# Performance work log

Hardware: AMD Instinct MI355X
Metric: run time of the kernel (lower is better)

## Reference

```python
import jax, jax.numpy as jnp
import numpy as np

B, T, N_EMBD = 1, 512, 768
N_HEAD, N_KV_HEAD = 12, 6
HEAD_DIM = N_EMBD // N_HEAD  # 64


def rms_norm(x, eps=1e-6):
    return x * jax.lax.rsqrt(jnp.mean(x * x, axis=-1, keepdims=True) + eps)


def apply_rotary_emb(x, cos, sin):
    # x: [B, T, H, D]; cos/sin: [T, D//2]
    d2 = x.shape[-1] // 2
    x1, x2 = x[..., :d2], x[..., d2:]
    c = cos[None, :, None, :]
    s = sin[None, :, None, :]
    return jnp.concatenate([x1 * c - x2 * s, x2 * c + x1 * s], axis=-1)


def tropical_dot_product(q, k):
    # q: [B,H,T,D], k: [B,H,S,D] -> max-plus score [B,H,T,S]
    return jnp.max(q[..., :, None, :] + k[..., None, :, :], axis=-1)


def setup_inputs() -> dict:
    key = jax.random.key(0)
    ks = jax.random.split(key, 5)
    x = jax.random.normal(ks[0], (B, T, N_EMBD), dtype=jnp.float32)
    # Real RoPE tables
    half = HEAD_DIM // 2
    inv_freq = 1.0 / (10000.0 ** (np.arange(0, half, dtype=np.float32) / half))
    t = np.arange(T, dtype=np.float32)
    freqs = np.outer(t, inv_freq)  # [T, D//2]
    cos = jnp.asarray(np.cos(freqs), dtype=jnp.float32)
    sin = jnp.asarray(np.sin(freqs), dtype=jnp.float32)
    std = 0.02
    Wq = std * jax.random.normal(ks[1], (N_EMBD, N_HEAD * HEAD_DIM), dtype=jnp.float32)
    Wk = std * jax.random.normal(ks[2], (N_EMBD, N_KV_HEAD * HEAD_DIM), dtype=jnp.float32)
    Wv = std * jax.random.normal(ks[3], (N_EMBD, N_KV_HEAD * HEAD_DIM), dtype=jnp.float32)
    Wproj = std * jax.random.normal(ks[4], (N_EMBD, N_EMBD), dtype=jnp.float32)
    return {"x": x, "cos": cos, "sin": sin, "Wq": Wq, "Wk": Wk, "Wv": Wv, "Wproj": Wproj}


def reference(x, cos, sin, Wq, Wk, Wv, Wproj):
    b, t, c = x.shape
    q = (x @ Wq).reshape(b, t, N_HEAD, HEAD_DIM)
    k = (x @ Wk).reshape(b, t, N_KV_HEAD, HEAD_DIM)
    v = (x @ Wv).reshape(b, t, N_KV_HEAD, HEAD_DIM)
    q = rms_norm(apply_rotary_emb(q, cos, sin))
    k = rms_norm(apply_rotary_emb(k, cos, sin))
    q = jnp.transpose(q, (0, 2, 1, 3))  # [B,H,T,D]
    k = jnp.transpose(k, (0, 2, 1, 3))  # [B,Hkv,T,D]
    v = jnp.transpose(v, (0, 2, 1, 3))
    n_rep = N_HEAD // N_KV_HEAD
    if n_rep > 1:
        k = jnp.repeat(k, n_rep, axis=1)
        v = jnp.repeat(v, n_rep, axis=1)
    scores = tropical_dot_product(q, k)  # [B,H,T,T]
    causal = jnp.tril(jnp.ones((t, t), dtype=jnp.bool_))
    scores = scores + jnp.where(causal, 0.0, -jnp.inf)
    attn = jax.nn.softmax(scores, axis=-1)
    y = jnp.einsum('bhqk,bhkd->bhqd', attn, v)
    y = jnp.transpose(y, (0, 2, 1, 3)).reshape(b, t, c)
    return y @ Wproj
```

## Files before the change

kernel.cpp:

```cpp
#include <hip/hip_runtime.h>
#include <hip/hip_bf16.h>
#include <math.h>

#define TT   512
#define CEMB 768
#define NH   12
#define NKV  6
#define HD   64
#define KVC  (NKV*HD)

typedef short short8 __attribute__((ext_vector_type(8)));
typedef float floatx4 __attribute__((ext_vector_type(4)));

__device__ __forceinline__ unsigned pack_bf16(float lo, float hi){
  __hip_bfloat162 h = __float22bfloat162_rn(make_float2(lo, hi));
  return *reinterpret_cast<unsigned*>(&h);
}
__device__ __forceinline__ unsigned short bf16_rn(float f){
  unsigned u = __float_as_uint(f);
  u += 0x7FFFu + ((u>>16)&1u);
  return (unsigned short)(u>>16);
}
__device__ __forceinline__ float bf16_to_f32(unsigned short u){
  return __uint_as_float(((unsigned)u) << 16);
}

__global__ void __launch_bounds__(256) gemm_qkv_mfma(
    const float* __restrict__ X,
    const float* __restrict__ Wq, const float* __restrict__ Wk, const float* __restrict__ Wv,
    const float* __restrict__ Wp,
    const float* __restrict__ cosb, const float* __restrict__ sinb,
    float* __restrict__ q, float* __restrict__ k, float* __restrict__ v,
    unsigned short* __restrict__ WpF){
  int bx = blockIdx.x;
  if (bx >= 192){
    int t0 = (bx-192)*256 + threadIdx.x;
    for(int g=0; g<8; ++g){
      int u  = g*9216 + t0;
      int kp = u / 192;
      int n4 = (u - kp*192)*4;
      int kk = kp*2;
      float4 w0 = *(const float4*)&Wp[(size_t)kk*CEMB + n4];
      float4 w1 = *(const float4*)&Wp[(size_t)(kk+1)*CEMB + n4];
      int ks = kk>>5, qq = (kk>>3)&3, j = kk&7;
      #pragma unroll
      for(int i=0;i<4;i++){
        int n = n4+i, ct = n>>4, r = n&15;
        *(unsigned*)&WpF[ (((size_t)(ct*24 + ks)*64 + qq*16 + r)<<3) + j ] =
          pack_bf16((&w0.x)[i], (&w1.x)[i]);
      }
    }
    return;
  }
  int mt = bx / 24, nt = bx % 24;
  const float* W; int ldb, bcol;
  if (nt < 12)      { W = Wq; ldb = CEMB; bcol = nt*64; }
  else if (nt < 18) { W = Wk; ldb = KVC;  bcol = (nt-12)*64; }
  else              { W = Wv; ldb = KVC;  bcol = (nt-18)*64; }

  __shared__ __align__(16) unsigned short Al[2][64][40];
  __shared__ __align__(16) unsigned short Bl[2][64][40];

  int tid = threadIdx.x;
  int am  = tid>>2,  akg = (tid&3)*8;
  int bkp = tid>>4,  bn4 = (tid&15)*4;
  int w = tid>>6, lane = tid&63, qq = lane>>4, r = lane&15;

  floatx4 acc[4];
  #pragma unroll
  for(int c=0;c<4;c++) acc[c] = (floatx4){0.f,0.f,0.f,0.f};

  const float* Ap = X + (size_t)(mt*64 + am)*CEMB + akg;
  const float* Bp = W + (size_t)(2*bkp)*ldb + bcol + bn4;

  float4 a0 = *(const float4*)(Ap);
  float4 a1 = *(const float4*)(Ap + 4);
  float4 b0 = *(const float4*)(Bp);
  float4 b1 = *(const float4*)(Bp + ldb);

  int buf = 0;
  for(int k0=0; k0<CEMB; k0+=32){
    unsigned p0 = pack_bf16(a0.x,a0.y), p1 = pack_bf16(a0.z,a0.w);
    unsigned p2 = pack_bf16(a1.x,a1.y), p3 = pack_bf16(a1.z,a1.w);
    *(uint4*)&Al[buf][am][akg] = make_uint4(p0,p1,p2,p3);
    #pragma unroll
    for(int i=0;i<4;i++)
      *(unsigned*)&Bl[buf][bn4+i][2*bkp] = pack_bf16((&b0.x)[i], (&b1.x)[i]);
    if (k0 + 32 < CEMB){
      a0 = *(const float4*)(Ap + k0+32);
      a1 = *(const float4*)(Ap + k0+36);
      b0 = *(const float4*)(Bp + (size_t)(k0+32)*ldb);
      b1 = *(const float4*)(Bp + (size_t)(k0+33)*ldb);
    }
    __syncthreads();
    short8 af = *(short8*)&Al[buf][w*16 + r][qq*8];
    #pragma unroll
    for(int c=0;c<4;c++){
      short8 bf = *(short8*)&Bl[buf][c*16 + r][qq*8];
      acc[c] = __builtin_amdgcn_mfma_f32_16x16x32_bf16(af, bf, acc[c], 0,0,0);
    }
    buf ^= 1;
  }

  #pragma unroll
  for(int reg=0; reg<4; ++reg){
    int t = mt*64 + w*16 + qq*4 + reg;
    if (nt < 18){
      float cs0 = cosb[t*32 + r],      sn0 = sinb[t*32 + r];
      float cs1 = cosb[t*32 + 16 + r], sn1 = sinb[t*32 + 16 + r];
      float x0 = acc[0][reg], x1 = acc[1][reg], x2 = acc[2][reg], x3 = acc[3][reg];
      float n0 = x0*cs0 - x2*sn0;
      float n1 = x1*cs1 - x3*sn1;
      float n2 = x2*cs0 + x0*sn0;
      float n3 = x3*cs1 + x1*sn1;
      float ss = n0*n0 + n1*n1 + n2*n2 + n3*n3;
      ss += __shfl_xor(ss,1); ss += __shfl_xor(ss,2);
      ss += __shfl_xor(ss,4); ss += __shfl_xor(ss,8);
      float sc = rsqrtf(ss*(1.0f/64.0f) + 1e-6f);
      float* dst = (nt < 12) ? (q + (size_t)t*CEMB + nt*64)
                             : (k + (size_t)t*KVC + (nt-12)*64);
      dst[r]    = n0*sc; dst[16+r] = n1*sc;
      dst[32+r] = n2*sc; dst[48+r] = n3*sc;
    } else {
      float* dst = v + (size_t)t*KVC + (nt-18)*64;
      dst[r]    = acc[0][reg]; dst[16+r] = acc[1][reg];
      dst[32+r] = acc[2][reg]; dst[48+r] = acc[3][reg];
    }
  }
}

__global__ void __launch_bounds__(256) attn_tile(const float* __restrict__ qn,
    const float* __restrict__ kn, const float* __restrict__ vr,
    unsigned short* __restrict__ part_acc, float2* __restrict__ part_ml){
  __shared__ float QPsh[64*68];
  __shared__ float Ksh[64*64];
  __shared__ float Vsh[64*64];

  int h   = blockIdx.y;
  int idx = blockIdx.x;
  int qt = 0, rem = idx;
  while (rem > qt){ rem -= (qt+1); ++qt; }
  int ct = rem;
  int t0 = ct*64;

  int kvh  = h >> 1;
  int w    = threadIdx.x >> 6;
  int lane = threadIdx.x & 63;
  int lg   = lane >> 4;
  int lc   = lane & 15;

  #pragma unroll
  for(int sub=0; sub<4; ++sub){
    int rr = w*16 + sub*4 + lg;
    int sw = ((lc ^ (rr>>2)) & 15)*4;
    *(float4*)&QPsh[rr*68 + lc*4] =
      *(const float4*)&qn[(size_t)(qt*64+rr)*CEMB + h*HD + lc*4];
    *(float4*)&Ksh[rr*64 + sw] =
      *(const float4*)&kn[(size_t)(t0+rr)*KVC + kvh*HD + lc*4];
    *(float4*)&Vsh[rr*64 + sw] =
      *(const float4*)&vr[(size_t)(t0+rr)*KVC + kvh*HD + lc*4];
  }
  __syncthreads();

  float s[4][4];
  #pragma unroll
  for(int r=0;r<4;r++)
    #pragma unroll
    for(int c=0;c<4;c++) s[r][c] = -INFINITY;

  #pragma unroll
  for(int dg=0; dg<16; ++dg){
    float4 k4[4], q4[4];
    int ksw = ((dg ^ lc)&15)*4;
    #pragma unroll
    for(int c=0;c<4;c++)
      k4[c] = *(const float4*)&Ksh[(lc*4+c)*64 + ksw];
    #pragma unroll
    for(int r=0;r<4;r++)
      q4[r] = *(const float4*)&QPsh[(w*16+lg*4+r)*68 + dg*4];
    #pragma unroll
    for(int r=0;r<4;r++)
      #pragma unroll
      for(int c=0;c<4;c++)
        s[r][c] = fmaxf(s[r][c],
                  fmaxf(fmaxf(q4[r].x + k4[c].x, q4[r].y + k4[c].y),
                        fmaxf(q4[r].z + k4[c].z, q4[r].w + k4[c].w)));
  }

  float mrow[4], lrow[4];
  #pragma unroll
  for(int r=0;r<4;r++){
    int i = qt*64 + w*16 + lg*4 + r;
    #pragma unroll
    for(int c=0;c<4;c++)
      if (t0 + lc*4 + c > i) s[r][c] = -INFINITY;
    float mt = fmaxf(fmaxf(s[r][0],s[r][1]), fmaxf(s[r][2],s[r][3]));
    mt = fmaxf(mt, __shfl_xor(mt,1));
    mt = fmaxf(mt, __shfl_xor(mt,2));
    mt = fmaxf(mt, __shfl_xor(mt,4));
    mt = fmaxf(mt, __shfl_xor(mt,8));
    float p0 = __expf(s[r][0]-mt), p1 = __expf(s[r][1]-mt);
    float p2 = __expf(s[r][2]-mt), p3 = __expf(s[r][3]-mt);
    float ps = p0+p1+p2+p3;
    ps += __shfl_xor(ps,1); ps += __shfl_xor(ps,2);
    ps += __shfl_xor(ps,4); ps += __shfl_xor(ps,8);
    mrow[r] = mt; lrow[r] = ps;
    *(float4*)&QPsh[(w*16+lg*4+r)*68 + lc*4] = make_float4(p0,p1,p2,p3);
  }
  __builtin_amdgcn_wave_barrier();

  float acc[4][4];
  #pragma unroll
  for(int r=0;r<4;r++)
    #pragma unroll
    for(int c=0;c<4;c++) acc[r][c] = 0.f;

  #pragma unroll
  for(int jg=0; jg<16; ++jg){
    float4 v4[4], p4[4];
    int vsw = ((lc ^ jg)&15)*4;
    #pragma unroll
    for(int jj=0;jj<4;jj++)
      v4[jj] = *(const float4*)&Vsh[(jg*4+jj)*64 + vsw];
    #pragma unroll
    for(int r=0;r<4;r++)
      p4[r] = *(const float4*)&QPsh[(w*16+lg*4+r)*68 + jg*4];
    #pragma unroll
    for(int r=0;r<4;r++)
      #pragma unroll
      for(int c=0;c<4;c++)
        acc[r][c] = fmaf(p4[r].x, (&v4[0].x)[c], fmaf(p4[r].y, (&v4[1].x)[c],
                    fmaf(p4[r].z, (&v4[2].x)[c], fmaf(p4[r].w, (&v4[3].x)[c], acc[r][c]))));
  }

  #pragma unroll
  for(int r=0;r<4;r++){
    int i = qt*64 + w*16 + lg*4 + r;
    int pidx = (h*TT + i)*8 + ct;
    *(uint2*)&part_acc[(size_t)pidx*64 + lc*4] =
      make_uint2(pack_bf16(acc[r][0],acc[r][1]), pack_bf16(acc[r][2],acc[r][3]));
    if (lc == 0) part_ml[pidx] = make_float2(mrow[r], lrow[r]);
  }
}

__global__ void __launch_bounds__(256) attn_reduce(const unsigned short* __restrict__ part_acc,
    const float2* __restrict__ part_ml, unsigned short* __restrict__ yF){
  int wid  = (blockIdx.x * blockDim.x + threadIdx.x) >> 6;
  int lane = threadIdx.x & 63;
  int h = wid >> 9;
  int i = wid & 511;
  int nch = (i >> 6) + 1;
  int base = (h*TT + i)*8;

  float2 mls[8]; float acs[8];
  #pragma unroll
  for(int c=0;c<8;c++){
    mls[c] = part_ml[base + c];
    acs[c] = bf16_to_f32(part_acc[(size_t)(base + c)*64 + lane]);
  }

  float m = -INFINITY, l = 0.f, a = 0.f;
  #pragma unroll
  for(int c=0;c<8;c++){
    if (c < nch){
      float m_new = fmaxf(m, mls[c].x);
      float sa  = __expf(m - m_new);
      float sc_ = __expf(mls[c].x - m_new);
      l = l*sa + mls[c].y*sc_;
      a = a*sa + acs[c]*sc_;
      m = m_new;
    }
  }
  float val = a / l;
  int s = i>>4, rr = i&15;
  int ks = h*2 + (lane>>5), q2 = (lane>>3)&3, j = lane&7;
  yF[ (((size_t)(s*24 + ks)*64 + q2*16 + rr)<<3) + j ] = bf16_rn(val);
}

__global__ void __launch_bounds__(256) gemm_proj_mfma(
    const unsigned short* __restrict__ yF, const unsigned short* __restrict__ WpF,
    float* __restrict__ out){
  int bx = blockIdx.x;
  int mt = bx / 24, ntH = bx % 24;
  int tid = threadIdx.x, w = tid>>6, lane = tid&63, qq = lane>>4, r = lane&15;
  int s = mt*4 + w;

  const short8* Af = (const short8*)yF  + (size_t)s*24*64 + lane;
  const short8* Bf = (const short8*)WpF + lane;

  floatx4 acc[2];
  acc[0] = (floatx4){0.f,0.f,0.f,0.f};
  acc[1] = (floatx4){0.f,0.f,0.f,0.f};

  short8 ac_ = Af[0];
  short8 bc_[2];
  #pragma unroll
  for(int c=0;c<2;c++) bc_[c] = Bf[(size_t)((ntH*2+c)*24)*64];

  for(int ks=0; ks<24; ++ks){
    short8 an; short8 bn[2];
    if (ks < 23){
      an = Af[(size_t)(ks+1)*64];
      #pragma unroll
      for(int c=0;c<2;c++) bn[c] = Bf[(size_t)((ntH*2+c)*24 + ks+1)*64];
    }
    #pragma unroll
    for(int c=0;c<2;c++)
      acc[c] = __builtin_amdgcn_mfma_f32_16x16x32_bf16(ac_, bc_[c], acc[c], 0,0,0);
    if (ks < 23){
      ac_ = an;
      #pragma unroll
      for(int c=0;c<2;c++) bc_[c] = bn[c];
    }
  }

  #pragma unroll
  for(int reg=0; reg<4; ++reg){
    int t = mt*64 + w*16 + qq*4 + reg;
    float* dst = out + (size_t)t*CEMB + ntH*32;
    #pragma unroll
    for(int c=0;c<2;c++)
      dst[c*16 + r] = acc[c][reg];
  }
}

extern "C" void kernel_launch(void* const* d_in, const int* in_sizes, int n_in,
                              void* d_out, int out_size, void* d_ws, size_t ws_size,
                              hipStream_t stream){
  const float* x    = (const float*)d_in[0];
  const float* cosb = (const float*)d_in[1];
  const float* sinb = (const float*)d_in[2];
  const float* Wq   = (const float*)d_in[3];
  const float* Wk   = (const float*)d_in[4];
  const float* Wv   = (const float*)d_in[5];
  const float* Wp   = (const float*)d_in[6];
  float* out = (float*)d_out;

  float* ws        = (float*)d_ws;
  float* q_raw     = ws;
  float* k_raw     = q_raw + (size_t)TT*CEMB;
  float* v_raw     = k_raw + (size_t)TT*KVC;
  unsigned short* part_acc = (unsigned short*)(v_raw + (size_t)TT*KVC);
  float2* part_ml  = (float2*)(part_acc + (size_t)NH*TT*8*64);
  unsigned short* WpF = (unsigned short*)(part_ml + (size_t)NH*TT*8);
  unsigned short* yF  = WpF + (size_t)48*24*64*8;

  gemm_qkv_mfma <<<dim3(228),   256, 0, stream>>>(x, Wq, Wk, Wv, Wp, cosb, sinb,
                                                  q_raw, k_raw, v_raw, WpF);
  attn_tile     <<<dim3(36,NH), 256, 0, stream>>>(q_raw, k_raw, v_raw, part_acc, part_ml);
  attn_reduce   <<<dim3(NH*TT/4), 256, 0, stream>>>(part_acc, part_ml, yF);
  gemm_proj_mfma<<<dim3(192),   256, 0, stream>>>(yF, WpF, out);
}
```

Measured before the change: 115.8 us.

## Split attention tiles to 32 query rows, use packed float2 math, deepen GEMM prefetch

The attention tile kernel now handles 32 query rows per block instead of 64, doubling the grid to 72x12 blocks for more parallelism on the causal triangle. It also rewrites the inner max-plus and PV loops with float2 vector types to encourage packed FP32 instructions. The QKV GEMM unrolls its double-buffered loop into two explicit steps with two register prefetch sets in flight. The projection GEMM gets a 3-deep register prefetch ring. The risks are reduced per-block work, which means more K/V reloads per query, and higher register pressure.

Result: no change. 116.1 us (+0.3%).

```diff
diff --git a/kernel.cpp b/kernel.cpp
--- a/kernel.cpp
+++ b/kernel.cpp
@@ -11,6 +11,7 @@
 
 typedef short short8 __attribute__((ext_vector_type(8)));
 typedef float floatx4 __attribute__((ext_vector_type(4)));
+typedef float floatx2 __attribute__((ext_vector_type(2)));
 
 __device__ __forceinline__ unsigned pack_bf16(float lo, float hi){
   __hip_bfloat162 h = __float22bfloat162_rn(make_float2(lo, hi));
@@ -73,33 +74,41 @@
   const float* Ap = X + (size_t)(mt*64 + am)*CEMB + akg;
   const float* Bp = W + (size_t)(2*bkp)*ldb + bcol + bn4;
 
-  float4 a0 = *(const float4*)(Ap);
-  float4 a1 = *(const float4*)(Ap + 4);
-  float4 b0 = *(const float4*)(Bp);
-  float4 b1 = *(const float4*)(Bp + ldb);
-
-  int buf = 0;
-  for(int k0=0; k0<CEMB; k0+=32){
-    unsigned p0 = pack_bf16(a0.x,a0.y), p1 = pack_bf16(a0.z,a0.w);
-    unsigned p2 = pack_bf16(a1.x,a1.y), p3 = pack_bf16(a1.z,a1.w);
-    *(uint4*)&Al[buf][am][akg] = make_uint4(p0,p1,p2,p3);
+  float4 a00 = *(const float4*)(Ap);
+  float4 a01 = *(const float4*)(Ap + 4);
+  float4 b00 = *(const float4*)(Bp);
+  float4 b01 = *(const float4*)(Bp + ldb);
+  float4 a10 = *(const float4*)(Ap + 32);
+  float4 a11 = *(const float4*)(Ap + 36);
+  float4 b10 = *(const float4*)(Bp + (size_t)32*ldb);
+  float4 b11 = *(const float4*)(Bp + (size_t)33*ldb);
+
+  auto step = [&](int k0, float4& A0, float4& A1, float4& B0, float4& B1,
+                  int bufc) {
+    unsigned p0 = pack_bf16(A0.x,A0.y), p1 = pack_bf16(A0.z,A0.w);
+    unsigned p2 = pack_bf16(A1.x,A1.y), p3 = pack_bf16(A1.z,A1.w);
+    *(uint4*)&Al[bufc][am][akg] = make_uint4(p0,p1,p2,p3);
     #pragma unroll
     for(int i=0;i<4;i++)
-      *(unsigned*)&Bl[buf][bn4+i][2*bkp] = pack_bf16((&b0.x)[i], (&b1.x)[i]);
-    if (k0 + 32 < CEMB){
-      a0 = *(const float4*)(Ap + k0+32);
-      a1 = *(const float4*)(Ap + k0+36);
-      b0 = *(const float4*)(Bp + (size_t)(k0+32)*ldb);
-      b1 = *(const float4*)(Bp + (size_t)(k0+33)*ldb);
+      *(unsigned*)&Bl[bufc][bn4+i][2*bkp] = pack_bf16((&B0.x)[i], (&B1.x)[i]);
+    if (k0 + 64 < CEMB){
+      A0 = *(const float4*)(Ap + k0+64);
+      A1 = *(const float4*)(Ap + k0+68);
+      B0 = *(const float4*)(Bp + (size_t)(k0+64)*ldb);
+      B1 = *(const float4*)(Bp + (size_t)(k0+65)*ldb);
     }
     __syncthreads();
-    short8 af = *(short8*)&Al[buf][w*16 + r][qq*8];
+    short8 af = *(short8*)&Al[bufc][w*16 + r][qq*8];
     #pragma unroll
     for(int c=0;c<4;c++){
-      short8 bf = *(short8*)&Bl[buf][c*16 + r][qq*8];
-      acc[c] = __builtin_amdgcn_mfma_f32_16x16x32_bf16(af, bf, acc[c], 0,0,0);
-    }
-    buf ^= 1;
+      short8 bfr = *(short8*)&Bl[bufc][c*16 + r][qq*8];
+      acc[c] = __builtin_amdgcn_mfma_f32_16x16x32_bf16(af, bfr, acc[c], 0,0,0);
+    }
+  };
+
+  for(int k0=0; k0<CEMB; k0+=64){
+    step(k0,    a00,a01,b00,b01, 0);
+    step(k0+32, a10,a11,b10,b11, 1);
   }
 
   #pragma unroll
@@ -132,29 +141,36 @@
 __global__ void __launch_bounds__(256) attn_tile(const float* __restrict__ qn,
     const float* __restrict__ kn, const float* __restrict__ vr,
     unsigned short* __restrict__ part_acc, float2* __restrict__ part_ml){
-  __shared__ float QPsh[64*68];
+  __shared__ float QPsh[32*68];
   __shared__ float Ksh[64*64];
   __shared__ float Vsh[64*64];
 
   int h   = blockIdx.y;
   int idx = blockIdx.x;
-  int qt = 0, rem = idx;
-  while (rem > qt){ rem -= (qt+1); ++qt; }
+  int qs = 0, rem = idx;
+  while (rem > (qs>>1)){ rem -= (qs>>1)+1; ++qs; }
   int ct = rem;
   int t0 = ct*64;
 
   int kvh  = h >> 1;
-  int w    = threadIdx.x >> 6;
-  int lane = threadIdx.x & 63;
+  int tid  = threadIdx.x;
+  int w    = tid >> 6;
+  int lane = tid & 63;
   int lg   = lane >> 4;
   int lc   = lane & 15;
 
+  {
+    int rr = tid >> 4;
+    int c4 = (tid & 15) * 4;
+    *(float4*)&QPsh[rr*68 + c4] =
+      *(const float4*)&qn[(size_t)(qs*32+rr)*CEMB + h*HD + c4];
+    *(float4*)&QPsh[(rr+16)*68 + c4] =
+      *(const float4*)&qn[(size_t)(qs*32+rr+16)*CEMB + h*HD + c4];
+  }
   #pragma unroll
   for(int sub=0; sub<4; ++sub){
     int rr = w*16 + sub*4 + lg;
     int sw = ((lc ^ (rr>>2)) & 15)*4;
-    *(float4*)&QPsh[rr*68 + lc*4] =
-      *(const float4*)&qn[(size_t)(qt*64+rr)*CEMB + h*HD + lc*4];
     *(float4*)&Ksh[rr*64 + sw] =
       *(const float4*)&kn[(size_t)(t0+rr)*KVC + kvh*HD + lc*4];
     *(float4*)&Vsh[rr*64 + sw] =
@@ -162,35 +178,41 @@
   }
   __syncthreads();
 
-  float s[4][4];
-  #pragma unroll
-  for(int r=0;r<4;r++)
+  float s[2][4];
+  #pragma unroll
+  for(int r=0;r<2;r++)
     #pragma unroll
     for(int c=0;c<4;c++) s[r][c] = -INFINITY;
 
   #pragma unroll
   for(int dg=0; dg<16; ++dg){
-    float4 k4[4], q4[4];
+    floatx2 ka[4], kb[4];
     int ksw = ((dg ^ lc)&15)*4;
     #pragma unroll
-    for(int c=0;c<4;c++)
-      k4[c] = *(const float4*)&Ksh[(lc*4+c)*64 + ksw];
-    #pragma unroll
-    for(int r=0;r<4;r++)
-      q4[r] = *(const float4*)&QPsh[(w*16+lg*4+r)*68 + dg*4];
-    #pragma unroll
-    for(int r=0;r<4;r++)
+    for(int c=0;c<4;c++){
+      float4 kv = *(const float4*)&Ksh[(lc*4+c)*64 + ksw];
+      ka[c] = (floatx2){kv.x, kv.y};
+      kb[c] = (floatx2){kv.z, kv.w};
+    }
+    #pragma unroll
+    for(int r=0;r<2;r++){
+      float4 qv = *(const float4*)&QPsh[(w*8+lg*2+r)*68 + dg*4];
+      floatx2 qa = (floatx2){qv.x, qv.y};
+      floatx2 qb = (floatx2){qv.z, qv.w};
       #pragma unroll
-      for(int c=0;c<4;c++)
+      for(int c=0;c<4;c++){
+        floatx2 sa = qa + ka[c];
+        floatx2 sb = qb + kb[c];
         s[r][c] = fmaxf(s[r][c],
-                  fmaxf(fmaxf(q4[r].x + k4[c].x, q4[r].y + k4[c].y),
-                        fmaxf(q4[r].z + k4[c].z, q4[r].w + k4[c].w)));
-  }
-
-  float mrow[4], lrow[4];
-  #pragma unroll
-  for(int r=0;r<4;r++){
-    int i = qt*64 + w*16 + lg*4 + r;
+                  fmaxf(fmaxf(sa.x, sa.y), fmaxf(sb.x, sb.y)));
+      }
+    }
+  }
+
+  float mrow[2], lrow[2];
+  #pragma unroll
+  for(int r=0;r<2;r++){
+    int i = qs*32 + w*8 + lg*2 + r;
     #pragma unroll
     for(int c=0;c<4;c++)
       if (t0 + lc*4 + c > i) s[r][c] = -INFINITY;
@@ -205,40 +227,47 @@
     ps += __shfl_xor(ps,1); ps += __shfl_xor(ps,2);
     ps += __shfl_xor(ps,4); ps += __shfl_xor(ps,8);
     mrow[r] = mt; lrow[r] = ps;
-    *(float4*)&QPsh[(w*16+lg*4+r)*68 + lc*4] = make_float4(p0,p1,p2,p3);
+    *(float4*)&QPsh[(w*8+lg*2+r)*68 + lc*4] = make_float4(p0,p1,p2,p3);
   }
   __builtin_amdgcn_wave_barrier();
 
-  float acc[4][4];
-  #pragma unroll
-  for(int r=0;r<4;r++)
-    #pragma unroll
-    for(int c=0;c<4;c++) acc[r][c] = 0.f;
+  floatx2 acc2[2][2];
+  #pragma unroll
+  for(int r=0;r<2;r++){
+    acc2[r][0] = (floatx2){0.f,0.f};
+    acc2[r][1] = (floatx2){0.f,0.f};
+  }
 
   #pragma unroll
   for(int jg=0; jg<16; ++jg){
-    float4 v4[4], p4[4];
+    floatx2 va[4], vb[4];
     int vsw = ((lc ^ jg)&15)*4;
     #pragma unroll
-    for(int jj=0;jj<4;jj++)
-      v4[jj] = *(const float4*)&Vsh[(jg*4+jj)*64 + vsw];
-    #pragma unroll
-    for(int r=0;r<4;r++)
-      p4[r] = *(const float4*)&QPsh[(w*16+lg*4+r)*68 + jg*4];
-    #pragma unroll
-    for(int r=0;r<4;r++)
+    for(int jj=0;jj<4;jj++){
+      float4 vv = *(const float4*)&Vsh[(jg*4+jj)*64 + vsw];
+      va[jj] = (floatx2){vv.x, vv.y};
+      vb[jj] = (floatx2){vv.z, vv.w};
+    }
+    #pragma unroll
+    for(int r=0;r<2;r++){
+      float4 pv = *(const float4*)&QPsh[(w*8+lg*2+r)*68 + jg*4];
       #pragma unroll
-      for(int c=0;c<4;c++)
-        acc[r][c] = fmaf(p4[r].x, (&v4[0].x)[c], fmaf(p4[r].y, (&v4[1].x)[c],
-                    fmaf(p4[r].z, (&v4[2].x)[c], fmaf(p4[r].w, (&v4[3].x)[c], acc[r][c]))));
-  }
-
-  #pragma unroll
-  for(int r=0;r<4;r++){
-    int i = qt*64 + w*16 + lg*4 + r;
+      for(int jj=0;jj<4;jj++){
+        float pj = (&pv.x)[jj];
+        floatx2 pp = (floatx2){pj, pj};
+        acc2[r][0] = __builtin_elementwise_fma(pp, va[jj], acc2[r][0]);
+        acc2[r][1] = __builtin_elementwise_fma(pp, vb[jj], acc2[r][1]);
+      }
+    }
+  }
+
+  #pragma unroll
+  for(int r=0;r<2;r++){
+    int i = qs*32 + w*8 + lg*2 + r;
     int pidx = (h*TT + i)*8 + ct;
     *(uint2*)&part_acc[(size_t)pidx*64 + lc*4] =
-      make_uint2(pack_bf16(acc[r][0],acc[r][1]), pack_bf16(acc[r][2],acc[r][3]));
+      make_uint2(pack_bf16(acc2[r][0].x, acc2[r][0].y),
+                 pack_bf16(acc2[r][1].x, acc2[r][1].y));
     if (lc == 0) part_ml[pidx] = make_float2(mrow[r], lrow[r]);
   }
 }
@@ -292,26 +321,26 @@
   acc[0] = (floatx4){0.f,0.f,0.f,0.f};
   acc[1] = (floatx4){0.f,0.f,0.f,0.f};
 
-  short8 ac_ = Af[0];
-  short8 bc_[2];
-  #pragma unroll
-  for(int c=0;c<2;c++) bc_[c] = Bf[(size_t)((ntH*2+c)*24)*64];
-
+  short8 ar[4]; short8 br[4][2];
+  #pragma unroll
+  for(int j=0;j<3;++j){
+    ar[j] = Af[(size_t)j*64];
+    #pragma unroll
+    for(int c=0;c<2;c++) br[j][c] = Bf[(size_t)((ntH*2+c)*24 + j)*64];
+  }
+
+  #pragma unroll
   for(int ks=0; ks<24; ++ks){
-    short8 an; short8 bn[2];
-    if (ks < 23){
-      an = Af[(size_t)(ks+1)*64];
+    int cur = ks & 3;
+    if (ks + 3 < 24){
+      int nx = (ks+3) & 3;
+      ar[nx] = Af[(size_t)(ks+3)*64];
       #pragma unroll
-      for(int c=0;c<2;c++) bn[c] = Bf[(size_t)((ntH*2+c)*24 + ks+1)*64];
+      for(int c=0;c<2;c++) br[nx][c] = Bf[(size_t)((ntH*2+c)*24 + ks+3)*64];
     }
     #pragma unroll
     for(int c=0;c<2;c++)
-      acc[c] = __builtin_amdgcn_mfma_f32_16x16x32_bf16(ac_, bc_[c], acc[c], 0,0,0);
-    if (ks < 23){
-      ac_ = an;
-      #pragma unroll
-      for(int c=0;c<2;c++) bc_[c] = bn[c];
-    }
+      acc[c] = __builtin_amdgcn_mfma_f32_16x16x32_bf16(ar[cur], br[cur][c], acc[c], 0,0,0);
   }
 
   #pragma unroll
@@ -347,7 +376,7 @@
 
   gemm_qkv_mfma <<<dim3(228),   256, 0, stream>>>(x, Wq, Wk, Wv, Wp, cosb, sinb,
                                                   q_raw, k_raw, v_raw, WpF);
-  attn_tile     <<<dim3(36,NH), 256, 0, stream>>>(q_raw, k_raw, v_raw, part_acc, part_ml);
+  attn_tile     <<<dim3(72,NH), 256, 0, stream>>>(q_raw, k_raw, v_raw, part_acc, part_ml);
   attn_reduce   <<<dim3(NH*TT/4), 256, 0, stream>>>(part_acc, part_ml, yF);
   gemm_proj_mfma<<<dim3(192),   256, 0, stream>>>(yF, WpF, out);
 }
```

## Deepen global-load prefetch in GEMMs and remap attention blocks across XCDs

Applied to the files above, without the earlier changes.

The QKV GEMM now keeps two register stages of global loads in flight, prefetching 64 columns ahead, with the loop unrolled by two over the LDS double buffer. The projection GEMM uses a 4-deep register ring that prefetches 3 k-steps ahead and fully unrolls the loop. Attention launches as a flat 1D grid whose block index is permuted (bid&7)*54 + (bid>>3), presumably so consecutive blocks of a head spread across the 8 XCDs. Together these aim to hide memory latency and balance the causal work, at the cost of more registers.

New measurement: 115.0 us. No clear change (-0.7%).

```diff
diff --git a/kernel.cpp b/kernel.cpp
--- a/kernel.cpp
+++ b/kernel.cpp
@@ -73,33 +73,41 @@
   const float* Ap = X + (size_t)(mt*64 + am)*CEMB + akg;
   const float* Bp = W + (size_t)(2*bkp)*ldb + bcol + bn4;
 
-  float4 a0 = *(const float4*)(Ap);
-  float4 a1 = *(const float4*)(Ap + 4);
-  float4 b0 = *(const float4*)(Bp);
-  float4 b1 = *(const float4*)(Bp + ldb);
-
-  int buf = 0;
-  for(int k0=0; k0<CEMB; k0+=32){
-    unsigned p0 = pack_bf16(a0.x,a0.y), p1 = pack_bf16(a0.z,a0.w);
-    unsigned p2 = pack_bf16(a1.x,a1.y), p3 = pack_bf16(a1.z,a1.w);
-    *(uint4*)&Al[buf][am][akg] = make_uint4(p0,p1,p2,p3);
+  float4 a00 = *(const float4*)(Ap);
+  float4 a01 = *(const float4*)(Ap + 4);
+  float4 b00 = *(const float4*)(Bp);
+  float4 b01 = *(const float4*)(Bp + ldb);
+  float4 a10 = *(const float4*)(Ap + 32);
+  float4 a11 = *(const float4*)(Ap + 36);
+  float4 b10 = *(const float4*)(Bp + (size_t)32*ldb);
+  float4 b11 = *(const float4*)(Bp + (size_t)33*ldb);
+
+  auto step = [&](int k0, float4& A0, float4& A1, float4& B0, float4& B1,
+                  int bufc) {
+    unsigned p0 = pack_bf16(A0.x,A0.y), p1 = pack_bf16(A0.z,A0.w);
+    unsigned p2 = pack_bf16(A1.x,A1.y), p3 = pack_bf16(A1.z,A1.w);
+    *(uint4*)&Al[bufc][am][akg] = make_uint4(p0,p1,p2,p3);
     #pragma unroll
     for(int i=0;i<4;i++)
-      *(unsigned*)&Bl[buf][bn4+i][2*bkp] = pack_bf16((&b0.x)[i], (&b1.x)[i]);
-    if (k0 + 32 < CEMB){
-      a0 = *(const float4*)(Ap + k0+32);
-      a1 = *(const float4*)(Ap + k0+36);
-      b0 = *(const float4*)(Bp + (size_t)(k0+32)*ldb);
-      b1 = *(const float4*)(Bp + (size_t)(k0+33)*ldb);
+      *(unsigned*)&Bl[bufc][bn4+i][2*bkp] = pack_bf16((&B0.x)[i], (&B1.x)[i]);
+    if (k0 + 64 < CEMB){
+      A0 = *(const float4*)(Ap + k0+64);
+      A1 = *(const float4*)(Ap + k0+68);
+      B0 = *(const float4*)(Bp + (size_t)(k0+64)*ldb);
+      B1 = *(const float4*)(Bp + (size_t)(k0+65)*ldb);
     }
     __syncthreads();
-    short8 af = *(short8*)&Al[buf][w*16 + r][qq*8];
+    short8 af = *(short8*)&Al[bufc][w*16 + r][qq*8];
     #pragma unroll
     for(int c=0;c<4;c++){
-      short8 bf = *(short8*)&Bl[buf][c*16 + r][qq*8];
-      acc[c] = __builtin_amdgcn_mfma_f32_16x16x32_bf16(af, bf, acc[c], 0,0,0);
-    }
-    buf ^= 1;
+      short8 bfr = *(short8*)&Bl[bufc][c*16 + r][qq*8];
+      acc[c] = __builtin_amdgcn_mfma_f32_16x16x32_bf16(af, bfr, acc[c], 0,0,0);
+    }
+  };
+
+  for(int k0=0; k0<CEMB; k0+=64){
+    step(k0,    a00,a01,b00,b01, 0);
+    step(k0+32, a10,a11,b10,b11, 1);
   }
 
   #pragma unroll
@@ -136,8 +144,10 @@
   __shared__ float Ksh[64*64];
   __shared__ float Vsh[64*64];
 
-  int h   = blockIdx.y;
-  int idx = blockIdx.x;
+  int bid = blockIdx.x;
+  int lin = (bid & 7)*54 + (bid >> 3);
+  int h   = lin / 36;
+  int idx = lin % 36;
   int qt = 0, rem = idx;
   while (rem > qt){ rem -= (qt+1); ++qt; }
   int ct = rem;
@@ -292,26 +302,26 @@
   acc[0] = (floatx4){0.f,0.f,0.f,0.f};
   acc[1] = (floatx4){0.f,0.f,0.f,0.f};
 
-  short8 ac_ = Af[0];
-  short8 bc_[2];
-  #pragma unroll
-  for(int c=0;c<2;c++) bc_[c] = Bf[(size_t)((ntH*2+c)*24)*64];
-
+  short8 ar[4]; short8 br[4][2];
+  #pragma unroll
+  for(int j=0;j<3;++j){
+    ar[j] = Af[(size_t)j*64];
+    #pragma unroll
+    for(int c=0;c<2;c++) br[j][c] = Bf[(size_t)((ntH*2+c)*24 + j)*64];
+  }
+
+  #pragma unroll
   for(int ks=0; ks<24; ++ks){
-    short8 an; short8 bn[2];
-    if (ks < 23){
-      an = Af[(size_t)(ks+1)*64];
+    int cur = ks & 3;
+    if (ks + 3 < 24){
+      int nx = (ks+3) & 3;
+      ar[nx] = Af[(size_t)(ks+3)*64];
       #pragma unroll
-      for(int c=0;c<2;c++) bn[c] = Bf[(size_t)((ntH*2+c)*24 + ks+1)*64];
+      for(int c=0;c<2;c++) br[nx][c] = Bf[(size_t)((ntH*2+c)*24 + ks+3)*64];
     }
     #pragma unroll
     for(int c=0;c<2;c++)
-      acc[c] = __builtin_amdgcn_mfma_f32_16x16x32_bf16(ac_, bc_[c], acc[c], 0,0,0);
-    if (ks < 23){
-      ac_ = an;
-      #pragma unroll
-      for(int c=0;c<2;c++) bc_[c] = bn[c];
-    }
+      acc[c] = __builtin_amdgcn_mfma_f32_16x16x32_bf16(ar[cur], br[cur][c], acc[c], 0,0,0);
   }
 
   #pragma unroll
@@ -347,7 +357,7 @@
 
   gemm_qkv_mfma <<<dim3(228),   256, 0, stream>>>(x, Wq, Wk, Wv, Wp, cosb, sinb,
                                                   q_raw, k_raw, v_raw, WpF);
-  attn_tile     <<<dim3(36,NH), 256, 0, stream>>>(q_raw, k_raw, v_raw, part_acc, part_ml);
+  attn_tile     <<<dim3(432),   256, 0, stream>>>(q_raw, k_raw, v_raw, part_acc, part_ml);
   attn_reduce   <<<dim3(NH*TT/4), 256, 0, stream>>>(part_acc, part_ml, yF);
   gemm_proj_mfma<<<dim3(192),   256, 0, stream>>>(yF, WpF, out);
 }
```
